# Performance work log

Hardware: AMD Instinct MI355X
Metric: run time of the kernel (lower is better)

The kernel has to match this reference:

```python
import jax, jax.numpy as jnp
from jax import lax
import numpy as np

# db3 analysis/synthesis filter bank (pywt coefficients)
DEC_LO = np.array([0.035226291882100656, -0.085441273882241486, -0.13501102001039084,
                   0.45987750211933132, 0.80689150931333875, 0.33267055295095688], dtype=np.float32)
DEC_HI = np.array([-0.33267055295095688, 0.80689150931333875, -0.45987750211933132,
                   -0.13501102001039084, 0.085441273882241486, 0.035226291882100656], dtype=np.float32)
REC_LO = DEC_LO[::-1].copy()
REC_HI = np.array([0.035226291882100656, 0.085441273882241486, -0.13501102001039084,
                   -0.45987750211933132, 0.80689150931333875, -0.33267055295095688], dtype=np.float32)
L = 6  # db3 filter length
DN = ('NCHW', 'OIHW', 'NCHW')

# analysis correlation kernels (torch conv2d correlates, pytorch_wavelets pre-flips dec filters)
H0_A = jnp.asarray(DEC_LO[::-1].copy())
H1_A = jnp.asarray(DEC_HI[::-1].copy())
# synthesis: conv_transpose(x, g, stride=2, pad=L-2) == correlate(dilate(x,2), flip(g), pad=1)
G0_S = jnp.asarray(REC_LO[::-1].copy())
G1_S = jnp.asarray(REC_HI[::-1].copy())


def _sep_conv(x, f, axis, stride=1, lhs_dil=1, pad=0):
    """Depthwise 1-D correlation along H (axis=2) or W (axis=3) of an NCHW tensor."""
    C = x.shape[1]
    if axis == 2:
        k = jnp.tile(f.reshape(1, 1, -1, 1), (C, 1, 1, 1))
        strides, dil, padding = (stride, 1), (lhs_dil, 1), ((pad, pad), (0, 0))
    else:
        k = jnp.tile(f.reshape(1, 1, 1, -1), (C, 1, 1, 1))
        strides, dil, padding = (1, stride), (1, lhs_dil), ((0, 0), (pad, pad))
    return lax.conv_general_dilated(x, k, strides, padding, lhs_dilation=dil,
                                    dimension_numbers=DN, feature_group_count=C)


def _dwt2(x):
    # single-level separable 2D DWT, mode='zero' (pytorch_wavelets: rows then cols)
    lo = _sep_conv(x, H0_A, 3, stride=2, pad=L - 2)
    hi = _sep_conv(x, H1_A, 3, stride=2, pad=L - 2)
    ll = _sep_conv(lo, H0_A, 2, stride=2, pad=L - 2)
    lh = _sep_conv(lo, H1_A, 2, stride=2, pad=L - 2)  # yh[:,:,0]
    hl = _sep_conv(hi, H0_A, 2, stride=2, pad=L - 2)  # yh[:,:,1]
    hh = _sep_conv(hi, H1_A, 2, stride=2, pad=L - 2)  # yh[:,:,2]
    return ll, lh, hl, hh


def _idwt2(ll, lh, hl, hh):
    # inverse: cols then rows; transposed conv realized as lhs_dilation=2 + pad 1
    lo = _sep_conv(ll, G0_S, 2, lhs_dil=2, pad=1) + _sep_conv(lh, G1_S, 2, lhs_dil=2, pad=1)
    hi = _sep_conv(hl, G0_S, 2, lhs_dil=2, pad=1) + _sep_conv(hh, G1_S, 2, lhs_dil=2, pad=1)
    return _sep_conv(lo, G0_S, 3, lhs_dil=2, pad=1) + _sep_conv(hi, G1_S, 3, lhs_dil=2, pad=1)


def _dw3x3(x, w):
    # depthwise 3x3, padding 1, no bias; w: (C,1,3,3)
    return lax.conv_general_dilated(x, w, (1, 1), ((1, 1), (1, 1)),
                                    dimension_numbers=DN, feature_group_count=x.shape[1])


def _ssl(x, conv5_w, conv7_w, conv9_w):
    # faithful to original: conv5 applied to BOTH yl and ylh; conv1/conv_cat unused
    ll, lh, hl, hh = _dwt2(x)
    return _idwt2(_dw3x3(ll, conv5_w), _dw3x3(lh, conv5_w),
                  _dw3x3(hl, conv7_w), _dw3x3(hh, conv9_w))


def setup_inputs() -> dict:
    key = jax.random.key(0)
    ks = jax.random.split(key, 7)
    B, C, H, W, HEADS = 4, 256, 192, 192, 8
    s = 0.05
    return {
        'x': jax.random.normal(ks[0], (B, C, H, W), jnp.float32),
        'qkv_w': jax.random.normal(ks[1], (2 * C, C), jnp.float32) * s,        # 1x1 conv C->2C
        'qkv_conv_w': jax.random.normal(ks[2], (2 * C, 1, 3, 3), jnp.float32) * s,  # depthwise 3x3
        'conv5_w': jax.random.normal(ks[3], (C, 1, 3, 3), jnp.float32) * s,
        'conv7_w': jax.random.normal(ks[4], (C, 1, 3, 3), jnp.float32) * s,
        'conv9_w': jax.random.normal(ks[5], (C, 1, 3, 3), jnp.float32) * s,
        'proj_w': jax.random.normal(ks[6], (C, C), jnp.float32) * s,           # 1x1 conv C->C
        'temperature': jnp.ones((1, HEADS, 1, 1), jnp.float32),
        'num_heads': HEADS,
    }


def reference(x, qkv_w, qkv_conv_w, conv5_w, conv7_w, conv9_w, proj_w, temperature, num_heads):
    b, c, h, w = x.shape
    eps = 1e-12
    kv = jnp.einsum('oc,bchw->bohw', qkv_w, x)          # 1x1 conv, no bias
    kv = _dw3x3(kv, qkv_conv_w)
    k, v = jnp.split(kv, 2, axis=1)
    q = _ssl(x, conv5_w, conv7_w, conv9_w)              # wavelet query path, same HxW
    d = c // num_heads
    q = q.reshape(b, num_heads, d, h * w)
    k = k.reshape(b, num_heads, d, h * w)
    v = v.reshape(b, num_heads, d, h * w)
    q = q / jnp.maximum(jnp.linalg.norm(q, axis=-1, keepdims=True), eps)
    k = k / jnp.maximum(jnp.linalg.norm(k, axis=-1, keepdims=True), eps)
    attn = jax.nn.softmax(jnp.einsum('bhdn,bhen->bhde', q, k) * temperature, axis=-1)  # (b,H,d,d)
    out = jnp.einsum('bhde,bhen->bhdn', attn, v).reshape(b, c, h, w)
    return jnp.einsum('oc,bchw->bohw', proj_w, out)
```

## Files before the change

### kernel.cpp

```cpp
#include <hip/hip_runtime.h>
#include <hip/hip_bf16.h>

typedef __hip_bfloat16 bf16;
typedef __attribute__((ext_vector_type(8))) short short8v;
typedef __attribute__((ext_vector_type(4))) float f32x4;

#define NB 4
#define NC 256
#define NPIX 36864
#define NH 192
#define NW 192
#define SW 98
#define SH 98
#define GCH 24

__device__ __constant__ float cH0A[6] = {  0.33267055295095688f,  0.80689150931333875f,  0.45987750211933132f, -0.13501102001039084f, -0.085441273882241486f, 0.035226291882100656f };
__device__ __constant__ float cH1A[6] = {  0.035226291882100656f, 0.085441273882241486f, -0.13501102001039084f, -0.45987750211933132f,  0.80689150931333875f, -0.33267055295095688f };
__device__ __constant__ float cG0S[6] = {  0.035226291882100656f, -0.085441273882241486f, -0.13501102001039084f, 0.45987750211933132f,  0.80689150931333875f,  0.33267055295095688f };
__device__ __constant__ float cG1S[6] = { -0.33267055295095688f,  0.80689150931333875f, -0.45987750211933132f, -0.13501102001039084f,  0.085441273882241486f, 0.035226291882100656f };

__device__ inline unsigned short bfbits(float f) {
    bf16 h = __float2bfloat16(f);
    return *reinterpret_cast<unsigned short*>(&h);
}
__device__ inline float b2f(short s) {
    return __bfloat162float(*reinterpret_cast<const bf16*>(&s));
}
__device__ inline short f2s(float f) {
    bf16 h = __float2bfloat16(f);
    return *reinterpret_cast<short*>(&h);
}

__global__ __launch_bounds__(256) void k_wave(const float* __restrict__ x,
                                              const float* __restrict__ w5, const float* __restrict__ w7,
                                              const float* __restrict__ w9,
                                              bf16* __restrict__ q, float* __restrict__ qsum) {
    int w0 = blockIdx.x * 64, h0 = blockIdx.y * 32;
    int bc = blockIdx.z;
    int c = bc & 255;
    int jh0 = h0 >> 1, jw0 = w0 >> 1;
    int xr0 = 2 * jh0 - 6;
    int xc0 = 2 * jw0 - 8;
    __shared__ float s_x[44][80];
    __shared__ short s_lo[44][38];
    __shared__ short s_hi[44][38];
    __shared__ short s_sub[4][20][38];
    __shared__ float s_c[4][18][34];
    __shared__ float s_lh[2][32][34];
    __shared__ float s_w[4][9];
    __shared__ float red[4];
    const float* xp = x + (size_t)bc * NPIX;
    int t = threadIdx.x;
    if (t < 36) {
        int f = t / 9, k = t - f * 9;
        const float* wsel = (f <= 1) ? w5 : (f == 2 ? w7 : w9);
        s_w[f][k] = wsel[c * 9 + k];
    }
    for (int e = t; e < 880; e += 256) {
        int r = e / 20, s = e - r * 20;
        int row = xr0 + r, col0 = xc0 + s * 4;
        float4 v = make_float4(0.f, 0.f, 0.f, 0.f);
        if (row >= 0 && row < NH) {
            if (col0 >= 0 && col0 + 3 < NW) {
                v = *reinterpret_cast<const float4*>(xp + (size_t)row * NW + col0);
            } else {
#pragma unroll
                for (int j = 0; j < 4; ++j) {
                    int cc = col0 + j;
                    if (cc >= 0 && cc < NW) (&v.x)[j] = xp[(size_t)row * NW + cc];
                }
            }
        }
        *reinterpret_cast<float4*>(&s_x[r][s * 4]) = v;
    }
    __syncthreads();
    for (int e = t; e < 1672; e += 256) {
        int r = e / 38, jc = e - r * 38;
        float la = 0.f, ha = 0.f;
#pragma unroll
        for (int tp = 0; tp < 6; ++tp) {
            float v = s_x[r][2 * jc + tp];
            la = fmaf(v, cH0A[tp], la);
            ha = fmaf(v, cH1A[tp], ha);
        }
        s_lo[r][jc] = f2s(la); s_hi[r][jc] = f2s(ha);
    }
    __syncthreads();
    for (int e = t; e < 760; e += 256) {
        int r = e / 38, jc = e - r * 38;
        int gr = jh0 - 1 + r, gcol = jw0 - 2 + jc;
        bool inb = (gr >= 0 && gr < SH && gcol >= 0 && gcol < SW);
        float ll = 0.f, lh = 0.f, hl = 0.f, hh = 0.f;
#pragma unroll
        for (int tp = 0; tp < 6; ++tp) {
            float lv = b2f(s_lo[2 * r + tp][jc]);
            float hv = b2f(s_hi[2 * r + tp][jc]);
            ll = fmaf(lv, cH0A[tp], ll); lh = fmaf(lv, cH1A[tp], lh);
            hl = fmaf(hv, cH0A[tp], hl); hh = fmaf(hv, cH1A[tp], hh);
        }
        s_sub[0][r][jc] = inb ? f2s(ll) : (short)0;
        s_sub[1][r][jc] = inb ? f2s(lh) : (short)0;
        s_sub[2][r][jc] = inb ? f2s(hl) : (short)0;
        s_sub[3][r][jc] = inb ? f2s(hh) : (short)0;
    }
    float ge0[3] = { cG0S[1], cG0S[3], cG0S[5] };
    float go0[3] = { cG0S[0], cG0S[2], cG0S[4] };
    float ge1[3] = { cG1S[1], cG1S[3], cG1S[5] };
    float go1[3] = { cG1S[0], cG1S[2], cG1S[4] };
    __syncthreads();
    for (int e = t; e < 2448; e += 256) {
        int pl = e / 612;
        int r2 = e - pl * 612;
        int r = r2 / 34, cc = r2 - r * 34;
        const float* wp = s_w[pl];
        float a = 0.f;
#pragma unroll
        for (int ky = 0; ky < 3; ++ky)
#pragma unroll
            for (int kx = 0; kx < 3; ++kx)
                a = fmaf(b2f(s_sub[pl][r + ky][cc + 1 + kx]), wp[ky * 3 + kx], a);
        s_c[pl][r][cc] = a;
    }
    __syncthreads();
    for (int e = t; e < 2176; e += 256) {
        int which = e / 1088;
        int r2 = e - which * 1088;
        int hh = r2 / 34, cc = r2 - hh * 34;
        int par = hh & 1;
        int j0 = hh >> 1;
        float a = 0.f;
#pragma unroll
        for (int i = 0; i < 3; ++i) {
            float g0 = par ? go0[i] : ge0[i];
            float g1 = par ? go1[i] : ge1[i];
            a = fmaf(s_c[2 * which][j0 + i][cc], g0, a);
            a = fmaf(s_c[2 * which + 1][j0 + i][cc], g1, a);
        }
        s_lh[which][hh][cc] = a;
    }
    __syncthreads();
    float lsum = 0.f;
    bf16* qp = q + (size_t)bc * NPIX;
#pragma unroll
    for (int it = 0; it < 8; ++it) {
        int e = t + 256 * it;
        int hh = e >> 6, ww = e & 63;
        int par = ww & 1;
        int j0 = ww >> 1;
        float a = 0.f;
#pragma unroll
        for (int i = 0; i < 3; ++i) {
            float g0 = par ? go0[i] : ge0[i];
            float g1 = par ? go1[i] : ge1[i];
            a = fmaf(s_lh[0][hh][j0 + i], g0, a);
            a = fmaf(s_lh[1][hh][j0 + i], g1, a);
        }
        qp[(size_t)(h0 + hh) * NW + w0 + ww] = __float2bfloat16(a);
        lsum = fmaf(a, a, lsum);
    }
#pragma unroll
    for (int off = 32; off; off >>= 1) lsum += __shfl_down(lsum, off, 64);
    if ((t & 63) == 0) red[t >> 6] = lsum;
    __syncthreads();
    if (t == 0) atomicAdd(&qsum[bc], red[0] + red[1] + red[2] + red[3]);
}

__global__ __launch_bounds__(256) void k_xpose(const float* __restrict__ x, bf16* __restrict__ xT) {
    __shared__ float T[64][68];
    int nt = blockIdx.x, ct = blockIdx.y, b = blockIdx.z;
    int n0 = nt * 64, c0 = ct * 64;
    const float* xb = x + ((size_t)b * NC + c0) * NPIX + n0;
    int t = threadIdx.x;
    int tr = t >> 4, tc4 = (t & 15) * 4;
#pragma unroll
    for (int i = 0; i < 4; ++i) {
        int cc = tr + i * 16;
        float4 v = *reinterpret_cast<const float4*>(xb + (size_t)cc * NPIX + tc4);
        T[cc][tc4] = v.x; T[cc][tc4 + 1] = v.y; T[cc][tc4 + 2] = v.z; T[cc][tc4 + 3] = v.w;
    }
    __syncthreads();
    bf16* ob = xT + ((size_t)b * NPIX + n0) * NC + c0;
#pragma unroll
    for (int i = 0; i < 4; ++i) {
        int nn = tr + i * 16;
        ushort4 u;
        u.x = bfbits(T[tc4][nn]); u.y = bfbits(T[tc4 + 1][nn]);
        u.z = bfbits(T[tc4 + 2][nn]); u.w = bfbits(T[tc4 + 3][nn]);
        *reinterpret_cast<ushort4*>(ob + (size_t)nn * NC + tc4) = u;
    }
}

__global__ __launch_bounds__(256) void k_cvtw(const float* __restrict__ w, bf16* __restrict__ wb) {
    int idx = blockIdx.x * 256 + threadIdx.x;
    if (idx < 512 * 256) wb[idx] = __float2bfloat16(w[idx]);
}

template <typename TOUT>
__global__ __launch_bounds__(256) void k_gemm_bf(const bf16* __restrict__ X, const bf16* __restrict__ Wm,
                                                 int wStride, TOUT* __restrict__ Out) {
    __shared__ __align__(16) short As[128 * 64];
    __shared__ __align__(16) short Bs[128 * 64];
    int nt = blockIdx.x, ot = blockIdx.y, b = blockIdx.z;
    int n0 = nt * 128, o0 = ot * 128;
    const bf16* xb = X + (size_t)b * NPIX * NC;
    const bf16* Wb = Wm + (size_t)b * wStride;
    int t = threadIdx.x;
    int wv = t >> 6, l = t & 63;
    int wr = wv >> 1, wc = wv & 1;
    f32x4 z4 = {0.f, 0.f, 0.f, 0.f};
    f32x4 acc[4][4];
#pragma unroll
    for (int m = 0; m < 4; ++m)
#pragma unroll
        for (int nf = 0; nf < 4; ++nf) acc[m][nf] = z4;
    for (int kc = 0; kc < 256; kc += 64) {
        __syncthreads();
#pragma unroll
        for (int i = 0; i < 4; ++i) {
            int blk = t + 256 * i;
            int r = blk >> 3, cb = blk & 7;
            int cbs = cb ^ (r & 7);
            *(short8v*)(As + r * 64 + cbs * 8) = *(const short8v*)(Wb + (size_t)(o0 + r) * NC + kc + cb * 8);
            *(short8v*)(Bs + r * 64 + cbs * 8) = *(const short8v*)(xb + (size_t)(n0 + r) * NC + kc + cb * 8);
        }
        __syncthreads();
#pragma unroll
        for (int kk = 0; kk < 2; ++kk) {
            int col8 = kk * 4 + (l >> 4);
            short8v av[4], bv[4];
#pragma unroll
            for (int m = 0; m < 4; ++m) {
                int row = wr * 64 + m * 16 + (l & 15);
                av[m] = *(const short8v*)(As + row * 64 + (col8 ^ (row & 7)) * 8);
            }
#pragma unroll
            for (int nf = 0; nf < 4; ++nf) {
                int row = wc * 64 + nf * 16 + (l & 15);
                bv[nf] = *(const short8v*)(Bs + row * 64 + (col8 ^ (row & 7)) * 8);
            }
#pragma unroll
            for (int m = 0; m < 4; ++m)
#pragma unroll
                for (int nf = 0; nf < 4; ++nf)
                    acc[m][nf] = __builtin_amdgcn_mfma_f32_16x16x32_bf16(av[m], bv[nf], acc[m][nf], 0, 0, 0);
        }
    }
    TOUT* ob = Out + (size_t)b * NC * NPIX;
#pragma unroll
    for (int m = 0; m < 4; ++m)
#pragma unroll
        for (int nf = 0; nf < 4; ++nf)
#pragma unroll
            for (int r = 0; r < 4; ++r) {
                int oo = o0 + wr * 64 + m * 16 + (l >> 4) * 4 + r;
                int nn = n0 + wc * 64 + nf * 16 + (l & 15);
                if constexpr (sizeof(TOUT) == 2)
                    ob[(size_t)oo * NPIX + nn] = __float2bfloat16(acc[m][nf][r]);
                else
                    ob[(size_t)oo * NPIX + nn] = acc[m][nf][r];
            }
}

__device__ inline short8v dw8(const bf16* __restrict__ chan, int r, int cb,
                              const float* __restrict__ w, float& ks) {
    float v[3][10];
#pragma unroll
    for (int ri = 0; ri < 3; ++ri) {
        int r2 = r + ri - 1;
        if (r2 < 0 || r2 >= NH) {
#pragma unroll
            for (int j = 0; j < 10; ++j) v[ri][j] = 0.f;
        } else {
            const bf16* p = chan + (size_t)r2 * NW + cb;
            short8v m = *(const short8v*)p;
            v[ri][0] = (cb > 0) ? __bfloat162float(p[-1]) : 0.f;
#pragma unroll
            for (int j = 0; j < 8; ++j) v[ri][j + 1] = b2f(m[j]);
            v[ri][9] = (cb < 184) ? __bfloat162float(p[8]) : 0.f;
        }
    }
    short8v out;
#pragma unroll
    for (int j = 0; j < 8; ++j) {
        float a = 0.f;
#pragma unroll
        for (int ri = 0; ri < 3; ++ri) {
            a = fmaf(v[ri][j],     w[ri * 3 + 0], a);
            a = fmaf(v[ri][j + 1], w[ri * 3 + 1], a);
            a = fmaf(v[ri][j + 2], w[ri * 3 + 2], a);
        }
        ks = fmaf(a, a, ks);
        out[j] = (short)bfbits(a);
    }
    return out;
}

__global__ __launch_bounds__(256) void k_gram_dw(const bf16* __restrict__ qbf, const bf16* __restrict__ kraw,
                                                 const float* __restrict__ dwW,
                                                 float* __restrict__ gpart, float* __restrict__ ksum) {
    int chunk = blockIdx.x;
    int bh = blockIdx.y; int b = bh >> 3, h = bh & 7;
    const bf16* qb = qbf + ((size_t)b * NC + h * 32) * NPIX;
    const bf16* kb = kraw + ((size_t)b * NC + h * 32) * NPIX;
    __shared__ float sg[4][1024];
    __shared__ float ksh[32];
    int t = threadIdx.x;
    int wv = t >> 6, l = t & 63;
    int dlo = l & 15, kslot = l >> 4;
    float wA[9], wB[9];
#pragma unroll
    for (int i = 0; i < 9; ++i) {
        wA[i] = dwW[(h * 32 + dlo) * 9 + i];
        wB[i] = dwW[(h * 32 + dlo + 16) * 9 + i];
    }
    const bf16* q0 = qb + (size_t)dlo * NPIX;
    const bf16* q1 = qb + (size_t)(dlo + 16) * NPIX;
    const bf16* k0 = kb + (size_t)dlo * NPIX;
    const bf16* k1 = kb + (size_t)(dlo + 16) * NPIX;
    f32x4 z4 = {0.f, 0.f, 0.f, 0.f};
    f32x4 a00 = z4, a01 = z4, a10 = z4, a11 = z4;
    float ks0 = 0.f, ks1 = 0.f;
    int r0 = chunk * 8 + wv * 2;
#pragma unroll
    for (int rr = 0; rr < 2; ++rr) {
        int r = r0 + rr;
#pragma unroll
        for (int c0 = 0; c0 < 192; c0 += 32) {
            int cb = c0 + kslot * 8;
            short8v av0 = *(const short8v*)(q0 + (size_t)r * NW + cb);
            short8v av1 = *(const short8v*)(q1 + (size_t)r * NW + cb);
            short8v bv0 = dw8(k0, r, cb, wA, ks0);
            short8v bv1 = dw8(k1, r, cb, wB, ks1);
            a00 = __builtin_amdgcn_mfma_f32_16x16x32_bf16(av0, bv0, a00, 0, 0, 0);
            a01 = __builtin_amdgcn_mfma_f32_16x16x32_bf16(av0, bv1, a01, 0, 0, 0);
            a10 = __builtin_amdgcn_mfma_f32_16x16x32_bf16(av1, bv0, a10, 0, 0, 0);
            a11 = __builtin_amdgcn_mfma_f32_16x16x32_bf16(av1, bv1, a11, 0, 0, 0);
        }
    }
    if (t < 32) ksh[t] = 0.f;
#pragma unroll
    for (int j = 0; j < 4; ++j) {
        int dA = kslot * 4 + j, dB = 16 + kslot * 4 + j;
        sg[wv][dA * 32 + dlo]      = a00[j];
        sg[wv][dA * 32 + 16 + dlo] = a01[j];
        sg[wv][dB * 32 + dlo]      = a10[j];
        sg[wv][dB * 32 + 16 + dlo] = a11[j];
    }
    __syncthreads();
    float* gp = gpart + ((size_t)bh * GCH + chunk) * 1024;
#pragma unroll
    for (int i = 0; i < 4; ++i) {
        int e = t + 256 * i;
        gp[e] = sg[0][e] + sg[1][e] + sg[2][e] + sg[3][e];
    }
    atomicAdd(&ksh[dlo], ks0);
    atomicAdd(&ksh[dlo + 16], ks1);
    __syncthreads();
    if (t < 32) atomicAdd(&ksum[b * NC + h * 32 + t], ksh[t]);
}

__global__ __launch_bounds__(1024) void k_attn(const float* __restrict__ gpart, const float* __restrict__ qsum,
                                               const float* __restrict__ ksum, const float* __restrict__ temp,
                                               float* __restrict__ attn) {
    int bh = blockIdx.x;
    int b = bh >> 3, h = bh & 7;
    int t = threadIdx.x;
    int d = t >> 5, e = t & 31;
    float s = 0.f;
    for (int i = 0; i < GCH; ++i) s += gpart[((size_t)bh * GCH + i) * 1024 + t];
    float rq = 1.f / fmaxf(sqrtf(qsum[b * NC + h * 32 + d]), 1e-12f);
    float rk = 1.f / fmaxf(sqrtf(ksum[b * NC + h * 32 + e]), 1e-12f);
    s *= rq * rk * temp[h];
    float m = s;
#pragma unroll
    for (int off = 16; off; off >>= 1) m = fmaxf(m, __shfl_xor(m, off, 32));
    float ex = expf(s - m);
    float sum = ex;
#pragma unroll
    for (int off = 16; off; off >>= 1) sum += __shfl_xor(sum, off, 32);
    attn[(size_t)bh * 1024 + t] = ex / sum;
}

__global__ __launch_bounds__(256) void k_wfold(const float* __restrict__ proj, const float* __restrict__ attn,
                                               bf16* __restrict__ wfbf) {
    int o = blockIdx.x, b = blockIdx.y;
    int t = threadIdx.x;
    int h = t >> 5, e = t & 31;
    const float* ap = attn + (size_t)(b * 8 + h) * 1024 + e;
    const float* pp = proj + o * NC + h * 32;
    float acc = 0.f;
#pragma unroll
    for (int d = 0; d < 32; ++d) acc = fmaf(pp[d], ap[d * 32], acc);
    wfbf[((size_t)b * NC + o) * NC + t] = __float2bfloat16(acc);
}

__global__ __launch_bounds__(256) void k_dwv(const bf16* __restrict__ vraw, const float* __restrict__ dwW,
                                             bf16* __restrict__ v2T) {
    int r = blockIdx.x;
    int cg = blockIdx.y;
    int b = blockIdx.z;
    __shared__ short s_v[3][32][204];
    const bf16* vb = vraw + ((size_t)b * NC + cg * 32) * NPIX;
    int t = threadIdx.x;
    for (int idx = t; idx < 4800; idx += 256) {
        int ri = idx / 1600;
        int rem = idx - ri * 1600;
        int e = rem / 50, j = rem - e * 50;
        int gr = r + ri - 1;
        int gc0 = -4 + 4 * j;
        ushort4 u = make_ushort4(0, 0, 0, 0);
        if (gr >= 0 && gr < NH && gc0 >= 0 && gc0 + 3 < NW)
            u = *reinterpret_cast<const ushort4*>(vb + (size_t)e * NPIX + (size_t)gr * NW + gc0);
        *reinterpret_cast<ushort4*>(&s_v[ri][e][4 * j]) = u;
    }
    int e = t & 31;
    int wslot = t >> 5;
    float w9[9];
#pragma unroll
    for (int i = 0; i < 9; ++i) w9[i] = dwW[(256 + cg * 32 + e) * 9 + i];
    __syncthreads();
    bf16* ob = v2T + ((size_t)b * NPIX + (size_t)r * NW) * NC + cg * 32 + e;
#pragma unroll
    for (int wi = 0; wi < 24; ++wi) {
        int w = wslot + 8 * wi;
        int cbase = w + 3;
        float a = 0.f;
#pragma unroll
        for (int ri = 0; ri < 3; ++ri) {
            a = fmaf(b2f(s_v[ri][e][cbase]),     w9[ri * 3 + 0], a);
            a = fmaf(b2f(s_v[ri][e][cbase + 1]), w9[ri * 3 + 1], a);
            a = fmaf(b2f(s_v[ri][e][cbase + 2]), w9[ri * 3 + 2], a);
        }
        ob[(size_t)w * NC] = __float2bfloat16(a);
    }
}


extern "C" void kernel_launch(void* const* d_in, const int* in_sizes, int n_in,
                              void* d_out, int out_size, void* d_ws, size_t ws_size,
                              hipStream_t stream) {
    (void)in_sizes; (void)n_in; (void)out_size;
    const float* x      = (const float*)d_in[0];
    const float* qkv_w  = (const float*)d_in[1];
    const float* qkv_cw = (const float*)d_in[2];
    const float* w5     = (const float*)d_in[3];
    const float* w7     = (const float*)d_in[4];
    const float* w9     = (const float*)d_in[5];
    const float* projw  = (const float*)d_in[6];
    const float* temp   = (const float*)d_in[7];

    const size_t OFF_SM    = 78675968;
    const size_t OFF_WBF   = OFF_SM;
    const size_t OFF_QSUM  = OFF_SM + 262144;
    const size_t OFF_KSUM  = OFF_QSUM + 4096;
    const size_t OFF_GPART = OFF_KSUM + 4096;
    const size_t OFF_ATTN  = OFF_GPART + 3145728;
    const size_t OFF_WF    = OFF_ATTN + 131072;
    const size_t WS_NEED   = OFF_WF + 524288;
    if (ws_size < WS_NEED) return;

    char* ws = (char*)d_ws;
    bf16*  kraw  = (bf16*)ws;
    bf16*  v2T   = (bf16*)ws;
    bf16*  wbf   = (bf16*)(ws + OFF_WBF);
    float* qsum  = (float*)(ws + OFF_QSUM);
    float* ksum  = (float*)(ws + OFF_KSUM);
    float* gpart = (float*)(ws + OFF_GPART);
    float* attn  = (float*)(ws + OFF_ATTN);
    bf16*  wfbf  = (bf16*)(ws + OFF_WF);

    bf16*  xbf  = (bf16*)d_out;
    bf16*  qbf  = (bf16*)((char*)d_out + 75497472);
    bf16*  vraw = (bf16*)((char*)d_out + 75497472);
    float* out  = (float*)d_out;

    hipMemsetAsync(ws + OFF_QSUM, 0, 8192, stream);

    k_wave<<<dim3(3, 6, NB * NC), 256, 0, stream>>>(x, w5, w7, w9, qbf, qsum);

    k_xpose<<<dim3(576, 4, NB), 256, 0, stream>>>(x, xbf);
    k_cvtw<<<512, 256, 0, stream>>>(qkv_w, wbf);

    k_gemm_bf<bf16><<<dim3(288, 2, NB), 256, 0, stream>>>(xbf, wbf, 0, kraw);
    k_gram_dw<<<dim3(GCH, 32), 256, 0, stream>>>(qbf, kraw, qkv_cw, gpart, ksum);

    k_attn<<<32, 1024, 0, stream>>>(gpart, qsum, ksum, temp, attn);
    k_wfold<<<dim3(256, NB), 256, 0, stream>>>(projw, attn, wfbf);

    k_gemm_bf<bf16><<<dim3(288, 2, NB), 256, 0, stream>>>(xbf, wbf + 256 * 256, 0, vraw);
    k_dwv<<<dim3(NH, 8, NB), 256, 0, stream>>>(vraw, qkv_cw, v2T);
    k_gemm_bf<float><<<dim3(288, 2, NB), 256, 0, stream>>>(v2T, wfbf, 65536, out);
}
```

Measured before the change: 594.3 us.

## Keep wavelet intermediates in fp32 shared memory, alias buffers, fuse even/odd synthesis

The wavelet query kernel now stores its intermediate subbands in fp32 instead of bf16, which removes the per-element conversions. It overlays the shared buffers in one aliased byte array so the block's shared footprint stays bounded. The inverse transform now has each thread compute both the even and odd polyphase outputs from shared loads it reuses, and the final stage writes two packed bf16 values per store. The cost is more shared memory per element, which may lower occupancy, and slightly different rounding in the intermediates.

```diff
diff --git a/kernel.cpp b/kernel.cpp
--- a/kernel.cpp
+++ b/kernel.cpp
@@ -26,10 +26,6 @@
 __device__ inline float b2f(short s) {
     return __bfloat162float(*reinterpret_cast<const bf16*>(&s));
 }
-__device__ inline short f2s(float f) {
-    bf16 h = __float2bfloat16(f);
-    return *reinterpret_cast<short*>(&h);
-}
 
 __global__ __launch_bounds__(256) void k_wave(const float* __restrict__ x,
                                               const float* __restrict__ w5, const float* __restrict__ w7,
@@ -39,14 +35,15 @@
     int bc = blockIdx.z;
     int c = bc & 255;
     int jh0 = h0 >> 1, jw0 = w0 >> 1;
-    int xr0 = 2 * jh0 - 6;
-    int xc0 = 2 * jw0 - 8;
-    __shared__ float s_x[44][80];
-    __shared__ short s_lo[44][38];
-    __shared__ short s_hi[44][38];
-    __shared__ short s_sub[4][20][38];
-    __shared__ float s_c[4][18][34];
-    __shared__ float s_lh[2][32][34];
+    int xr0 = h0 - 6;
+    int xc0 = w0 - 8;
+    __shared__ __align__(16) char smem[40320];
+    float (*s_x)[80]   = (float(*)[80])smem;
+    float (*s_c)[36]   = (float(*)[36])smem;
+    float (*s_lo)[40]  = (float(*)[40])(smem + 14080);
+    float (*s_hi)[40]  = (float(*)[40])(smem + 21120);
+    float (*s_lh)[36]  = (float(*)[36])(smem + 14080);
+    float (*s_sub)[38] = (float(*)[38])(smem + 28160);
     __shared__ float s_w[4][9];
     __shared__ float red[4];
     const float* xp = x + (size_t)bc * NPIX;
@@ -83,7 +80,7 @@
             la = fmaf(v, cH0A[tp], la);
             ha = fmaf(v, cH1A[tp], ha);
         }
-        s_lo[r][jc] = f2s(la); s_hi[r][jc] = f2s(ha);
+        s_lo[r][jc] = la; s_hi[r][jc] = ha;
     }
     __syncthreads();
     for (int e = t; e < 760; e += 256) {
@@ -93,70 +90,62 @@
         float ll = 0.f, lh = 0.f, hl = 0.f, hh = 0.f;
 #pragma unroll
         for (int tp = 0; tp < 6; ++tp) {
-            float lv = b2f(s_lo[2 * r + tp][jc]);
-            float hv = b2f(s_hi[2 * r + tp][jc]);
+            float lv = s_lo[2 * r + tp][jc];
+            float hv = s_hi[2 * r + tp][jc];
             ll = fmaf(lv, cH0A[tp], ll); lh = fmaf(lv, cH1A[tp], lh);
             hl = fmaf(hv, cH0A[tp], hl); hh = fmaf(hv, cH1A[tp], hh);
         }
-        s_sub[0][r][jc] = inb ? f2s(ll) : (short)0;
-        s_sub[1][r][jc] = inb ? f2s(lh) : (short)0;
-        s_sub[2][r][jc] = inb ? f2s(hl) : (short)0;
-        s_sub[3][r][jc] = inb ? f2s(hh) : (short)0;
-    }
-    float ge0[3] = { cG0S[1], cG0S[3], cG0S[5] };
-    float go0[3] = { cG0S[0], cG0S[2], cG0S[4] };
-    float ge1[3] = { cG1S[1], cG1S[3], cG1S[5] };
-    float go1[3] = { cG1S[0], cG1S[2], cG1S[4] };
+        s_sub[r][jc]      = inb ? ll : 0.f;
+        s_sub[20 + r][jc] = inb ? lh : 0.f;
+        s_sub[40 + r][jc] = inb ? hl : 0.f;
+        s_sub[60 + r][jc] = inb ? hh : 0.f;
+    }
     __syncthreads();
     for (int e = t; e < 2448; e += 256) {
-        int pl = e / 612;
-        int r2 = e - pl * 612;
-        int r = r2 / 34, cc = r2 - r * 34;
+        int pr = e / 34, cc = e - pr * 34;
+        int pl = pr / 18, r = pr - pl * 18;
         const float* wp = s_w[pl];
+        const int rb = pl * 20 + r;
         float a = 0.f;
 #pragma unroll
         for (int ky = 0; ky < 3; ++ky)
 #pragma unroll
             for (int kx = 0; kx < 3; ++kx)
-                a = fmaf(b2f(s_sub[pl][r + ky][cc + 1 + kx]), wp[ky * 3 + kx], a);
-        s_c[pl][r][cc] = a;
-    }
-    __syncthreads();
-    for (int e = t; e < 2176; e += 256) {
-        int which = e / 1088;
-        int r2 = e - which * 1088;
-        int hh = r2 / 34, cc = r2 - hh * 34;
-        int par = hh & 1;
-        int j0 = hh >> 1;
-        float a = 0.f;
-#pragma unroll
-        for (int i = 0; i < 3; ++i) {
-            float g0 = par ? go0[i] : ge0[i];
-            float g1 = par ? go1[i] : ge1[i];
-            a = fmaf(s_c[2 * which][j0 + i][cc], g0, a);
-            a = fmaf(s_c[2 * which + 1][j0 + i][cc], g1, a);
-        }
-        s_lh[which][hh][cc] = a;
+                a = fmaf(s_sub[rb + ky][cc + 1 + kx], wp[ky * 3 + kx], a);
+        s_c[pr][cc] = a;
+    }
+    __syncthreads();
+    for (int e = t; e < 1088; e += 256) {
+        int row = e / 34, cc = e - row * 34;
+        int which = row >> 4, m = row & 15;
+        float c0_0 = s_c[which * 36 + m][cc],     c1_0 = s_c[which * 36 + 18 + m][cc];
+        float c0_1 = s_c[which * 36 + m + 1][cc], c1_1 = s_c[which * 36 + 18 + m + 1][cc];
+        float c0_2 = s_c[which * 36 + m + 2][cc], c1_2 = s_c[which * 36 + 18 + m + 2][cc];
+        float ae = c0_0 * cG0S[1] + c0_1 * cG0S[3] + c0_2 * cG0S[5]
+                 + c1_0 * cG1S[1] + c1_1 * cG1S[3] + c1_2 * cG1S[5];
+        float ao = c0_0 * cG0S[0] + c0_1 * cG0S[2] + c0_2 * cG0S[4]
+                 + c1_0 * cG1S[0] + c1_1 * cG1S[2] + c1_2 * cG1S[4];
+        s_lh[which * 32 + 2 * m][cc] = ae;
+        s_lh[which * 32 + 2 * m + 1][cc] = ao;
     }
     __syncthreads();
     float lsum = 0.f;
     bf16* qp = q + (size_t)bc * NPIX;
 #pragma unroll
-    for (int it = 0; it < 8; ++it) {
+    for (int it = 0; it < 4; ++it) {
         int e = t + 256 * it;
-        int hh = e >> 6, ww = e & 63;
-        int par = ww & 1;
-        int j0 = ww >> 1;
-        float a = 0.f;
-#pragma unroll
-        for (int i = 0; i < 3; ++i) {
-            float g0 = par ? go0[i] : ge0[i];
-            float g1 = par ? go1[i] : ge1[i];
-            a = fmaf(s_lh[0][hh][j0 + i], g0, a);
-            a = fmaf(s_lh[1][hh][j0 + i], g1, a);
-        }
-        qp[(size_t)(h0 + hh) * NW + w0 + ww] = __float2bfloat16(a);
-        lsum = fmaf(a, a, lsum);
+        int hh = e >> 5, m = e & 31;
+        float l0 = s_lh[hh][m],     h0v = s_lh[32 + hh][m];
+        float l1 = s_lh[hh][m + 1], h1v = s_lh[32 + hh][m + 1];
+        float l2 = s_lh[hh][m + 2], h2v = s_lh[32 + hh][m + 2];
+        float ae = l0 * cG0S[1] + l1 * cG0S[3] + l2 * cG0S[5]
+                 + h0v * cG1S[1] + h1v * cG1S[3] + h2v * cG1S[5];
+        float ao = l0 * cG0S[0] + l1 * cG0S[2] + l2 * cG0S[4]
+                 + h0v * cG1S[0] + h1v * cG1S[2] + h2v * cG1S[4];
+        unsigned pack = (unsigned)bfbits(ae) | ((unsigned)bfbits(ao) << 16);
+        *reinterpret_cast<unsigned*>(qp + (size_t)(h0 + hh) * NW + w0 + 2 * m) = pack;
+        lsum = fmaf(ae, ae, lsum);
+        lsum = fmaf(ao, ao, lsum);
     }
 #pragma unroll
     for (int off = 32; off; off >>= 1) lsum += __shfl_down(lsum, off, 64);
```

New measurement: 536.6 us. 9.7% less time.
